# Kernel optimization log

Hardware: AMD Instinct MI355X
Metric: run time of the kernel (lower is better)

The kernel has to match this reference:

```python
import jax, jax.numpy as jnp
import numpy as np

D_MODEL = 1024
N_HEADS = 16
DIM_HEAD = D_MODEL // N_HEADS
SCALE = DIM_HEAD ** (-0.5)
B, T = 8, 1024


def setup_inputs() -> dict:
    key = jax.random.key(0)
    k1, k2, k3 = jax.random.split(key, 3)
    x = jax.random.normal(k1, (B, T, D_MODEL), dtype=jnp.float32)
    m = jnp.ones((B, T), dtype=jnp.float32)  # padding mask (1 = keep)
    w_qkv = jax.random.normal(k2, (3 * D_MODEL, D_MODEL), dtype=jnp.float32) * (D_MODEL ** -0.5)
    w_out = jax.random.normal(k3, (D_MODEL, D_MODEL), dtype=jnp.float32) * (D_MODEL ** -0.5)
    b_out = jnp.zeros((D_MODEL,), dtype=jnp.float32)
    return {"x": x, "m": m, "w_qkv": w_qkv, "w_out": w_out, "b_out": b_out, "l": T}


def reference(x, m, w_qkv, w_out, b_out, l):
    b, t, dm = x.shape
    qkv = jnp.einsum('btd,ed->bte', x, w_qkv)  # (b,t,3*d_model)
    q, k, v = jnp.split(qkv, 3, axis=-1)
    rs = lambda a: a.reshape(b, t, N_HEADS, DIM_HEAD)
    q, k, v = rs(q), rs(k), rs(v)
    e = jnp.einsum('bihd,bjhd->bijh', q, k) * SCALE  # (b,i,j,h)
    # combined padding + causal mask
    kpm = m[:, :, None] * m[:, None, :]              # (b,i,j)
    kpm = jnp.tril(kpm)[..., None]                   # (b,i,j,1)
    neg = -jnp.finfo(e.dtype).max
    e = jnp.where(kpm == 0, neg, e)
    a = jax.nn.softmax(e, axis=2)                    # softmax over j
    o = jnp.einsum('bijh,bjhd->bihd', a, v).reshape(b, t, dm)
    o = jnp.einsum('btd,ed->bte', o, w_out) + b_out
    # dropout is identity in eval mode
    return o * m[..., None]
```

## Files before the change

### kernel.cpp

```cpp
#include <hip/hip_runtime.h>
#include <cstdint>
#include <cstddef>

typedef unsigned short u16;
typedef __bf16 bf16;
typedef bf16 __attribute__((ext_vector_type(2))) bf16x2;
typedef bf16 __attribute__((ext_vector_type(8))) bf16x8;
typedef float __attribute__((ext_vector_type(4))) f32x4;
typedef u16 __attribute__((ext_vector_type(8))) u16x8;

#define QSCALE 0.18033688011112042f

__device__ __forceinline__ u16 f2b(float x) {
  unsigned u = __float_as_uint(x);
  unsigned r = (u + 0x7fffu + ((u >> 16) & 1u)) >> 16;
  return (u16)r;
}

__device__ __forceinline__ void gl_lds16(const void* g, void* lds) {
  __builtin_amdgcn_global_load_lds(
      (const __attribute__((address_space(1))) unsigned int*)g,
      (__attribute__((address_space(3))) unsigned int*)lds, 16, 0, 0);
}

__device__ __forceinline__ bf16x8 frag(const u16* base, int row, int kchunk) {
  const int c = kchunk ^ (row & 7);
  return *(const bf16x8*)(base + row * 64 + c * 8);
}
__device__ __forceinline__ void stage_tile4(const u16* gbase, int K, char* lbase,
                                            int wave, int lane) {
#pragma unroll
  for (int i = 0; i < 4; ++i) {
    const int q = wave * 64 + lane + i * 256;
    const int r = q >> 3, c = (q & 7) ^ (r & 7);
    gl_lds16(gbase + (size_t)r * K + c * 8, lbase + i * 4096 + wave * 1024);
  }
}

__device__ __forceinline__ bf16x8 frag32(const u16* base, int row, int kchunk) {
  const int c = kchunk ^ ((row >> 1) & 3);
  return *(const bf16x8*)(base + row * 32 + c * 8);
}
__device__ __forceinline__ void stage32(const u16* gbase, int K, char* lbase,
                                        int wave, int lane) {
  const int q0 = wave * 64 + lane;
  const int r0 = q0 >> 2, c0 = (q0 & 3) ^ ((r0 >> 1) & 3);
  gl_lds16(gbase + (size_t)r0 * K + c0 * 8, lbase + wave * 1024);
  const int q1 = q0 + 256;
  const int r1 = q1 >> 2, c1 = (q1 & 3) ^ ((r1 >> 1) & 3);
  gl_lds16(gbase + (size_t)r1 * K + c1 * 8, lbase + 4096 + wave * 1024);
}

__global__ __launch_bounds__(256) void castk(const float* __restrict__ in,
                                             u16* __restrict__ out, int n) {
  int i = (blockIdx.x * 256 + threadIdx.x) * 8;
  if (i >= n) return;
  float4 a = *(const float4*)(in + i);
  float4 b = *(const float4*)(in + i + 4);
  u16x8 v;
  v[0] = f2b(a.x); v[1] = f2b(a.y); v[2] = f2b(a.z); v[3] = f2b(a.w);
  v[4] = f2b(b.x); v[5] = f2b(b.y); v[6] = f2b(b.z); v[7] = f2b(b.w);
  *(u16x8*)(out + i) = v;
}

__global__ __launch_bounds__(256, 3) void gemm_qkv(
    const u16* __restrict__ A, const u16* __restrict__ B,
    u16* __restrict__ Qo, u16* __restrict__ Ko, u16* __restrict__ Vo) {
  __shared__ u16 As[3][128 * 32];
  __shared__ u16 Bs[3][128 * 32];
  const int tid = threadIdx.x;
  const int lane = tid & 63, wave = tid >> 6;
  const int fr = lane & 15, fg = lane >> 4;
  const int wr = wave >> 1, wc = wave & 1;
  const int bid = blockIdx.x;
  const int bm = bid & 63, bn = bid >> 6;
  const int K = 1024;
  const u16* Ab = A + (size_t)bm * 128 * K;
  const u16* Bb = B + (size_t)bn * 128 * K;

  f32x4 acc[4][4] = {};

  stage32(Ab, K, (char*)&As[0][0], wave, lane);
  stage32(Bb, K, (char*)&Bs[0][0], wave, lane);
  stage32(Ab + 32, K, (char*)&As[1][0], wave, lane);
  stage32(Bb + 32, K, (char*)&Bs[1][0], wave, lane);

  int cur = 0;
#pragma unroll 1
  for (int t = 0; t < 32; ++t) {
    if (t == 31) asm volatile("s_waitcnt vmcnt(0) lgkmcnt(0)" ::: "memory");
    else         asm volatile("s_waitcnt vmcnt(4) lgkmcnt(0)" ::: "memory");
    __builtin_amdgcn_s_barrier();
    __builtin_amdgcn_sched_barrier(0);
    if (t + 2 < 32) {
      int stg = cur + 2; if (stg >= 3) stg -= 3;
      stage32(Ab + (size_t)(t + 2) * 32, K, (char*)&As[stg][0], wave, lane);
      stage32(Bb + (size_t)(t + 2) * 32, K, (char*)&Bs[stg][0], wave, lane);
    }
    bf16x8 af[4], bfv[4];
#pragma unroll
    for (int mi = 0; mi < 4; ++mi)
      af[mi] = frag32(&As[cur][0], wr * 64 + mi * 16 + fr, fg);
#pragma unroll
    for (int ni = 0; ni < 4; ++ni)
      bfv[ni] = frag32(&Bs[cur][0], wc * 64 + ni * 16 + fr, fg);
#pragma unroll
    for (int mi = 0; mi < 4; ++mi)
#pragma unroll
      for (int ni = 0; ni < 4; ++ni)
        acc[mi][ni] = __builtin_amdgcn_mfma_f32_16x16x32_bf16(
            af[mi], bfv[ni], acc[mi][ni], 0, 0, 0);
    cur = (cur + 1 == 3) ? 0 : cur + 1;
  }

  const int gr0 = bm * 128 + wr * 64;
  const int gc0 = bn * 128 + wc * 64;
#pragma unroll
  for (int mi = 0; mi < 4; ++mi) {
    const int rb = gr0 + mi * 16 + fg * 4;
    const int b = rb >> 10, t = rb & 1023;
#pragma unroll
    for (int ni = 0; ni < 4; ++ni) {
      const int c = gc0 + ni * 16 + fr;
      const int region = c >> 10, cc = c & 1023;
      const int h = cc >> 6, d = cc & 63;
      const size_t bh = (size_t)(b * 16 + h);
      if (region == 0) {
#pragma unroll
        for (int g = 0; g < 4; ++g)
          Qo[(bh * 1024 + t + g) * 64 + d] = f2b(acc[mi][ni][g] * QSCALE);
      } else if (region == 1) {
#pragma unroll
        for (int g = 0; g < 4; ++g)
          Ko[(bh * 1024 + t + g) * 64 + d] = f2b(acc[mi][ni][g]);
      } else {
        ushort4 pv;
        pv.x = f2b(acc[mi][ni][0]);
        pv.y = f2b(acc[mi][ni][1]);
        pv.z = f2b(acc[mi][ni][2]);
        pv.w = f2b(acc[mi][ni][3]);
        *(ushort4*)(Vo + (bh * 64 + d) * 1024 + t) = pv;
      }
    }
  }
}

__global__ __launch_bounds__(256) void gemm_bt2(
    const u16* __restrict__ A, const u16* __restrict__ B,
    float* __restrict__ Co, const float* __restrict__ bias,
    const float* __restrict__ msk) {
  __shared__ u16 As[2][128 * 64];
  __shared__ u16 Bs[2][128 * 64];
  const int tid = threadIdx.x;
  const int lane = tid & 63, wave = tid >> 6;
  const int fr = lane & 15, fg = lane >> 4;
  const int wr = wave >> 1, wc = wave & 1;
  const int bid = blockIdx.x;
  const int bm = bid & 63, bn = bid >> 6;
  const int K = 1024, N = 1024;
  const u16* Ab = A + (size_t)bm * 128 * K;
  const u16* Bb = B + (size_t)bn * 128 * K;

  f32x4 acc[4][4] = {};

  stage_tile4(Ab, K, (char*)&As[0][0], wave, lane);
  stage_tile4(Bb, K, (char*)&Bs[0][0], wave, lane);
  __syncthreads();

  int cur = 0;
#pragma unroll 1
  for (int t = 0; t < 16; ++t) {
    if (t < 15) {
      stage_tile4(Ab + (size_t)(t + 1) * 64, K, (char*)&As[cur ^ 1][0], wave, lane);
      stage_tile4(Bb + (size_t)(t + 1) * 64, K, (char*)&Bs[cur ^ 1][0], wave, lane);
    }
    bf16x8 af[4][2], bfv[4][2];
#pragma unroll
    for (int mi = 0; mi < 4; ++mi)
#pragma unroll
      for (int kk = 0; kk < 2; ++kk)
        af[mi][kk] = frag(&As[cur][0], wr * 64 + mi * 16 + fr, kk * 4 + fg);
#pragma unroll
    for (int ni = 0; ni < 4; ++ni)
#pragma unroll
      for (int kk = 0; kk < 2; ++kk)
        bfv[ni][kk] = frag(&Bs[cur][0], wc * 64 + ni * 16 + fr, kk * 4 + fg);
#pragma unroll
    for (int mi = 0; mi < 4; ++mi)
#pragma unroll
      for (int ni = 0; ni < 4; ++ni)
#pragma unroll
        for (int kk = 0; kk < 2; ++kk)
          acc[mi][ni] = __builtin_amdgcn_mfma_f32_16x16x32_bf16(
              af[mi][kk], bfv[ni][kk], acc[mi][ni], 0, 0, 0);
    __syncthreads();
    cur ^= 1;
  }

  const int gr0 = bm * 128 + wr * 64;
  const int gc0 = bn * 128 + wc * 64;
#pragma unroll
  for (int mi = 0; mi < 4; ++mi) {
    const int rb = gr0 + mi * 16 + fg * 4;
#pragma unroll
    for (int ni = 0; ni < 4; ++ni) {
      const int c = gc0 + ni * 16 + fr;
      const float bo = bias[c];
#pragma unroll
      for (int g = 0; g < 4; ++g) {
        const int r = rb + g;
        Co[(size_t)r * N + c] = (acc[mi][ni][g] + bo) * msk[r];
      }
    }
  }
}

__global__ __launch_bounds__(256) void attnk(const u16* __restrict__ Qb,
                                             const u16* __restrict__ Kb,
                                             const u16* __restrict__ Vtb,
                                             const float* __restrict__ msk,
                                             u16* __restrict__ Ob) {
  __shared__ u16 Ks[2][64 * 64];
  __shared__ u16 Vs[2][64 * 64];
  __shared__ float mlds[1024];
  __shared__ int allone;
  const int tid = threadIdx.x;
  const int lane = tid & 63, wave = tid >> 6;
  const int fr = lane & 15, fg = lane >> 4;
  const int bid = blockIdx.x;
  const int s = bid >> 7;
  const int bh = bid & 127;
  const int b = bh >> 4, h = bh & 15;

  const float4 mv = ((const float4*)(msk + (size_t)b * 1024))[tid];
  ((float4*)mlds)[tid] = mv;
  if (tid == 0) allone = 1;
  __syncthreads();
  if (mv.x != 1.f || mv.y != 1.f || mv.z != 1.f || mv.w != 1.f) allone = 0;

  auto stage = [&](int kb, int buf) {
    const int q0 = wave * 64 + lane;
    const int r0 = q0 >> 3, c0 = (q0 & 7) ^ (r0 & 7);
    gl_lds16(Kb + ((size_t)bh * 1024 + kb * 64 + r0) * 64 + c0 * 8,
             (char*)&Ks[buf][0] + wave * 1024);
    gl_lds16(Vtb + ((size_t)bh * 64 + r0) * 1024 + kb * 64 + c0 * 8,
             (char*)&Vs[buf][0] + wave * 1024);
    const int q1 = q0 + 256;
    const int r1 = q1 >> 3, c1 = (q1 & 7) ^ (r1 & 7);
    gl_lds16(Kb + ((size_t)bh * 1024 + kb * 64 + r1) * 64 + c1 * 8,
             (char*)&Ks[buf][0] + 4096 + wave * 1024);
    gl_lds16(Vtb + ((size_t)bh * 64 + r1) * 1024 + kb * 64 + c1 * 8,
             (char*)&Vs[buf][0] + 4096 + wave * 1024);
  };

  int qw = s * 64 + wave * 16;
  bf16x8 qf[2];
  auto loadQ = [&]() {
#pragma unroll
    for (int kc = 0; kc < 2; ++kc)
      qf[kc] = *(const bf16x8*)(Qb + ((size_t)bh * 1024 + qw + fr) * 64 +
                                kc * 32 + fg * 8);
  };
  loadQ();

  f32x4 o[4] = {};
  float mrun = -3.0e38f, lrun = 0.f;

  auto writeO = [&]() {
    const float inv = 1.0f / lrun;
#pragma unroll
    for (int g = 0; g < 4; ++g) {
      const float invr = __shfl(inv, fg * 4 + g);
      const int q = qw + fg * 4 + g;
#pragma unroll
      for (int dt = 0; dt < 4; ++dt)
        Ob[((size_t)b * 1024 + q) * 1024 + h * 64 + dt * 16 + fr] =
            f2b(o[dt][g] * invr);
    }
  };

  stage(0, 0);

#pragma unroll 1
  for (int it = 0; it <= 16; ++it) {
    __syncthreads();
    const bool mfast = __builtin_amdgcn_readfirstlane(allone) != 0;
    if (it < 16) {
      const int nkb = (it + 1 <= s) ? (it + 1) : (it - s);
      stage(nkb, (it + 1) & 1);
    }
    if (it == s + 1) {
      writeO();
      qw = (15 - s) * 64 + wave * 16;
      loadQ();
#pragma unroll
      for (int dt = 0; dt < 4; ++dt) o[dt] = f32x4{0.f, 0.f, 0.f, 0.f};
      mrun = -3.0e38f;
      lrun = 0.f;
    }
    const int kb = (it <= s) ? it : (it - s - 1);
    const u16* Kc = &Ks[it & 1][0];
    const u16* Vc = &Vs[it & 1][0];

    f32x4 st[4];
    const f32x4 z = {0.f, 0.f, 0.f, 0.f};
    bf16x8 kf0[4], kf1[4];
#pragma unroll
    for (int nt = 0; nt < 4; ++nt) {
      const int krow = nt * 16 + fr;
      const int cb0r = (0 * 4 + fg) ^ (krow & 7);
      const int cb1r = (1 * 4 + fg) ^ (krow & 7);
      kf0[nt] = *(const bf16x8*)(Kc + krow * 64 + cb0r * 8);
      kf1[nt] = *(const bf16x8*)(Kc + krow * 64 + cb1r * 8);
    }
    __builtin_amdgcn_s_setprio(1);
#pragma unroll
    for (int nt = 0; nt < 4; ++nt) {
      st[nt] = __builtin_amdgcn_mfma_f32_16x16x32_bf16(kf0[nt], qf[0], z, 0, 0, 0);
      st[nt] = __builtin_amdgcn_mfma_f32_16x16x32_bf16(kf1[nt], qf[1], st[nt], 0, 0, 0);
    }
    __builtin_amdgcn_s_setprio(0);

    if (kb * 64 + 63 > qw) {
      const int q = qw + fr;
#pragma unroll
      for (int nt = 0; nt < 4; ++nt)
#pragma unroll
        for (int g = 0; g < 4; ++g) {
          const int j = kb * 64 + nt * 16 + fg * 4 + g;
          if (j > q) st[nt][g] = -3.0e38f;
        }
    }

    float mx = st[0][0];
#pragma unroll
    for (int nt = 0; nt < 4; ++nt)
#pragma unroll
      for (int g = 0; g < 4; ++g) mx = fmaxf(mx, st[nt][g]);
    mx = fmaxf(mx, __shfl_xor(mx, 16));
    mx = fmaxf(mx, __shfl_xor(mx, 32));
    float nm, sc;
    int doR;
    if (__all(mx <= mrun + 8.f)) {
      nm = mrun; sc = 1.f; doR = 0;
    } else {
      nm = fmaxf(mrun, mx);
      sc = exp2f(mrun - nm);
      mrun = nm; doR = 1;
    }
    float rs = 0.f;
    if (mfast) {
#pragma unroll
      for (int nt = 0; nt < 4; ++nt)
#pragma unroll
        for (int g = 0; g < 4; ++g) {
          const float pq = exp2f(st[nt][g] - nm);
          st[nt][g] = pq;
          rs += pq;
        }
    } else {
      float kmv[4][4];
#pragma unroll
      for (int nt = 0; nt < 4; ++nt) {
        const float4 km4 = *(const float4*)(&mlds[kb * 64 + nt * 16 + fg * 4]);
        kmv[nt][0] = km4.x; kmv[nt][1] = km4.y; kmv[nt][2] = km4.z; kmv[nt][3] = km4.w;
      }
#pragma unroll
      for (int nt = 0; nt < 4; ++nt)
#pragma unroll
        for (int g = 0; g < 4; ++g) {
          const float pq = exp2f(st[nt][g] - nm) * kmv[nt][g];
          st[nt][g] = pq;
          rs += pq;
        }
    }
    rs += __shfl_xor(rs, 16);
    rs += __shfl_xor(rs, 32);
    lrun = doR ? (lrun * sc + rs) : (lrun + rs);

    int pk[4][2];
#pragma unroll
    for (int nt = 0; nt < 4; ++nt)
#pragma unroll
      for (int hh = 0; hh < 2; ++hh) {
        bf16x2 tp;
        tp[0] = (bf16)st[nt][2 * hh];
        tp[1] = (bf16)st[nt][2 * hh + 1];
        pk[nt][hh] = __builtin_bit_cast(int, tp);
      }

    bf16x8 pa[2];
#pragma unroll
    for (int jc = 0; jc < 2; ++jc) {
      int w[4];
#pragma unroll
      for (int e2 = 0; e2 < 4; ++e2) {
        const int sl = fr + ((fg & 1) << 5) + ((e2 & 2) ? 16 : 0);
        const int lo = __shfl(pk[jc * 2 + 0][e2 & 1], sl);
        const int hi = __shfl(pk[jc * 2 + 1][e2 & 1], sl);
        w[e2] = (fg & 2) ? hi : lo;
      }
      int4 wi = {w[0], w[1], w[2], w[3]};
      pa[jc] = __builtin_bit_cast(bf16x8, wi);
    }

    if (doR) {
#pragma unroll
      for (int g = 0; g < 4; ++g) {
        const float scr = __shfl(sc, fg * 4 + g);
#pragma unroll
        for (int dt = 0; dt < 4; ++dt) o[dt][g] *= scr;
      }
    }

    __builtin_amdgcn_s_setprio(1);
#pragma unroll
    for (int jc = 0; jc < 2; ++jc)
#pragma unroll
      for (int dt = 0; dt < 4; ++dt) {
        const int vrow = dt * 16 + fr;
        const int cb = (jc * 4 + fg) ^ (vrow & 7);
        const bf16x8 vf = *(const bf16x8*)(Vc + vrow * 64 + cb * 8);
        o[dt] = __builtin_amdgcn_mfma_f32_16x16x32_bf16(pa[jc], vf, o[dt], 0, 0, 0);
      }
    __builtin_amdgcn_s_setprio(0);
  }

  writeO();
}

extern "C" void kernel_launch(void* const* d_in, const int* in_sizes, int n_in,
                              void* d_out, int out_size, void* d_ws, size_t ws_size,
                              hipStream_t stream) {
  (void)in_sizes; (void)n_in; (void)out_size; (void)ws_size;
  const float* x = (const float*)d_in[0];
  const float* m = (const float*)d_in[1];
  const float* w_qkv = (const float*)d_in[2];
  const float* w_out = (const float*)d_in[3];
  const float* b_out = (const float*)d_in[4];
  float* out = (float*)d_out;

  char* ws = (char*)d_ws;
  const size_t MB = 1u << 20;
  u16* Xb    = (u16*)(ws + 0);
  u16* Wqkvb = (u16*)(ws + 16 * MB);
  u16* Woutb = (u16*)(ws + 22 * MB);
  u16* Qb    = (u16*)(ws + 24 * MB);
  u16* Kb    = (u16*)(ws + 40 * MB);
  u16* Vtb   = (u16*)(ws + 56 * MB);
  u16* Ob    = Xb;

  castk<<<4096, 256, 0, stream>>>(x, Xb, 8 * 1024 * 1024);
  castk<<<1536, 256, 0, stream>>>(w_qkv, Wqkvb, 3072 * 1024);
  castk<<<512, 256, 0, stream>>>(w_out, Woutb, 1024 * 1024);

  gemm_qkv<<<1536, 256, 0, stream>>>(Xb, Wqkvb, Qb, Kb, Vtb);

  attnk<<<1024, 256, 0, stream>>>(Qb, Kb, Vtb, m, Ob);

  gemm_bt2<<<512, 256, 0, stream>>>(Ob, Woutb, out, b_out, m);
}
```

Baseline: 155.4 us.

## Merge cast kernels, enlarge QKV GEMM tile to 256x256, defer attention max shuffle

Three separate fp32-to-bf16 cast launches become one kernel that dispatches on block index, removing two launches. The QKV projection GEMM goes from 128x128 tiles with 256 threads to 256x256 tiles with 512 threads, giving more operand reuse per LDS load and fewer blocks (384). In attention, the cross-lane max reduction is skipped when every lane's local max stays within the threshold of the running max. The larger GEMM tile raises accumulator registers and LDS per block, which may lower occupancy. With only 384 blocks there may also be tail imbalance across CUs.

```diff
diff --git a/kernel.cpp b/kernel.cpp
--- a/kernel.cpp
+++ b/kernel.cpp
@@ -41,20 +41,21 @@
   const int c = kchunk ^ ((row >> 1) & 3);
   return *(const bf16x8*)(base + row * 32 + c * 8);
 }
-__device__ __forceinline__ void stage32(const u16* gbase, int K, char* lbase,
-                                        int wave, int lane) {
-  const int q0 = wave * 64 + lane;
-  const int r0 = q0 >> 2, c0 = (q0 & 3) ^ ((r0 >> 1) & 3);
-  gl_lds16(gbase + (size_t)r0 * K + c0 * 8, lbase + wave * 1024);
-  const int q1 = q0 + 256;
-  const int r1 = q1 >> 2, c1 = (q1 & 3) ^ ((r1 >> 1) & 3);
-  gl_lds16(gbase + (size_t)r1 * K + c1 * 8, lbase + 4096 + wave * 1024);
-}
-
-__global__ __launch_bounds__(256) void castk(const float* __restrict__ in,
-                                             u16* __restrict__ out, int n) {
-  int i = (blockIdx.x * 256 + threadIdx.x) * 8;
-  if (i >= n) return;
+
+__global__ __launch_bounds__(256) void castk3(const float* __restrict__ x,
+                                              const float* __restrict__ wq,
+                                              const float* __restrict__ wo,
+                                              u16* __restrict__ xb,
+                                              u16* __restrict__ wqb,
+                                              u16* __restrict__ wob) {
+  const int blk = blockIdx.x;
+  const float* in;
+  u16* out;
+  int base;
+  if (blk < 4096)      { in = x;  out = xb;  base = blk; }
+  else if (blk < 5632) { in = wq; out = wqb; base = blk - 4096; }
+  else                 { in = wo; out = wob; base = blk - 5632; }
+  const int i = (base * 256 + threadIdx.x) * 8;
   float4 a = *(const float4*)(in + i);
   float4 b = *(const float4*)(in + i + 4);
   u16x8 v;
@@ -63,27 +64,36 @@
   *(u16x8*)(out + i) = v;
 }
 
-__global__ __launch_bounds__(256, 3) void gemm_qkv(
+__global__ __launch_bounds__(512, 2) void gemm_qkv(
     const u16* __restrict__ A, const u16* __restrict__ B,
     u16* __restrict__ Qo, u16* __restrict__ Ko, u16* __restrict__ Vo) {
-  __shared__ u16 As[3][128 * 32];
-  __shared__ u16 Bs[3][128 * 32];
+  __shared__ u16 As[3][256 * 32];
+  __shared__ u16 Bs[3][256 * 32];
   const int tid = threadIdx.x;
   const int lane = tid & 63, wave = tid >> 6;
   const int fr = lane & 15, fg = lane >> 4;
-  const int wr = wave >> 1, wc = wave & 1;
+  const int wm = wave >> 2, wn = wave & 3;
   const int bid = blockIdx.x;
-  const int bm = bid & 63, bn = bid >> 6;
+  const int bm = bid & 31, bn = bid >> 5;
   const int K = 1024;
-  const u16* Ab = A + (size_t)bm * 128 * K;
-  const u16* Bb = B + (size_t)bn * 128 * K;
-
-  f32x4 acc[4][4] = {};
-
-  stage32(Ab, K, (char*)&As[0][0], wave, lane);
-  stage32(Bb, K, (char*)&Bs[0][0], wave, lane);
-  stage32(Ab + 32, K, (char*)&As[1][0], wave, lane);
-  stage32(Bb + 32, K, (char*)&Bs[1][0], wave, lane);
+  const u16* Ab = A + (size_t)bm * 256 * K;
+  const u16* Bb = B + (size_t)bn * 256 * K;
+
+  f32x4 acc[8][4] = {};
+
+  auto stage = [&](const u16* gbase, char* lbase) {
+    const int q0 = wave * 64 + lane;
+    const int r0 = q0 >> 2, c0 = (q0 & 3) ^ ((r0 >> 1) & 3);
+    gl_lds16(gbase + (size_t)r0 * K + c0 * 8, lbase + wave * 1024);
+    const int q1 = q0 + 512;
+    const int r1 = q1 >> 2, c1 = (q1 & 3) ^ ((r1 >> 1) & 3);
+    gl_lds16(gbase + (size_t)r1 * K + c1 * 8, lbase + 8192 + wave * 1024);
+  };
+
+  stage(Ab, (char*)&As[0][0]);
+  stage(Bb, (char*)&Bs[0][0]);
+  stage(Ab + 32, (char*)&As[1][0]);
+  stage(Bb + 32, (char*)&Bs[1][0]);
 
   int cur = 0;
 #pragma unroll 1
@@ -94,29 +104,28 @@
     __builtin_amdgcn_sched_barrier(0);
     if (t + 2 < 32) {
       int stg = cur + 2; if (stg >= 3) stg -= 3;
-      stage32(Ab + (size_t)(t + 2) * 32, K, (char*)&As[stg][0], wave, lane);
-      stage32(Bb + (size_t)(t + 2) * 32, K, (char*)&Bs[stg][0], wave, lane);
-    }
-    bf16x8 af[4], bfv[4];
-#pragma unroll
-    for (int mi = 0; mi < 4; ++mi)
-      af[mi] = frag32(&As[cur][0], wr * 64 + mi * 16 + fr, fg);
+      stage(Ab + (size_t)(t + 2) * 32, (char*)&As[stg][0]);
+      stage(Bb + (size_t)(t + 2) * 32, (char*)&Bs[stg][0]);
+    }
+    bf16x8 bfv[4];
 #pragma unroll
     for (int ni = 0; ni < 4; ++ni)
-      bfv[ni] = frag32(&Bs[cur][0], wc * 64 + ni * 16 + fr, fg);
-#pragma unroll
-    for (int mi = 0; mi < 4; ++mi)
+      bfv[ni] = frag32(&Bs[cur][0], wn * 64 + ni * 16 + fr, fg);
+#pragma unroll
+    for (int mi = 0; mi < 8; ++mi) {
+      const bf16x8 af = frag32(&As[cur][0], wm * 128 + mi * 16 + fr, fg);
 #pragma unroll
       for (int ni = 0; ni < 4; ++ni)
         acc[mi][ni] = __builtin_amdgcn_mfma_f32_16x16x32_bf16(
-            af[mi], bfv[ni], acc[mi][ni], 0, 0, 0);
+            af, bfv[ni], acc[mi][ni], 0, 0, 0);
+    }
     cur = (cur + 1 == 3) ? 0 : cur + 1;
   }
 
-  const int gr0 = bm * 128 + wr * 64;
-  const int gc0 = bn * 128 + wc * 64;
-#pragma unroll
-  for (int mi = 0; mi < 4; ++mi) {
+  const int gr0 = bm * 256 + wm * 128;
+  const int gc0 = bn * 256 + wn * 64;
+#pragma unroll
+  for (int mi = 0; mi < 8; ++mi) {
     const int rb = gr0 + mi * 16 + fg * 4;
     const int b = rb >> 10, t = rb & 1023;
 #pragma unroll
@@ -332,18 +341,18 @@
         }
     }
 
-    float mx = st[0][0];
+    float mxl = st[0][0];
 #pragma unroll
     for (int nt = 0; nt < 4; ++nt)
 #pragma unroll
-      for (int g = 0; g < 4; ++g) mx = fmaxf(mx, st[nt][g]);
-    mx = fmaxf(mx, __shfl_xor(mx, 16));
-    mx = fmaxf(mx, __shfl_xor(mx, 32));
+      for (int g = 0; g < 4; ++g) mxl = fmaxf(mxl, st[nt][g]);
     float nm, sc;
     int doR;
-    if (__all(mx <= mrun + 8.f)) {
+    if (__all(mxl <= mrun + 8.f)) {
       nm = mrun; sc = 1.f; doR = 0;
     } else {
+      float mx = fmaxf(mxl, __shfl_xor(mxl, 16));
+      mx = fmaxf(mx, __shfl_xor(mx, 32));
       nm = fmaxf(mrun, mx);
       sc = exp2f(mrun - nm);
       mrun = nm; doR = 1;
@@ -450,11 +459,9 @@
   u16* Vtb   = (u16*)(ws + 56 * MB);
   u16* Ob    = Xb;
 
-  castk<<<4096, 256, 0, stream>>>(x, Xb, 8 * 1024 * 1024);
-  castk<<<1536, 256, 0, stream>>>(w_qkv, Wqkvb, 3072 * 1024);
-  castk<<<512, 256, 0, stream>>>(w_out, Woutb, 1024 * 1024);
-
-  gemm_qkv<<<1536, 256, 0, stream>>>(Xb, Wqkvb, Qb, Kb, Vtb);
+  castk3<<<6144, 256, 0, stream>>>(x, w_qkv, w_out, Xb, Wqkvb, Woutb);
+
+  gemm_qkv<<<384, 512, 0, stream>>>(Xb, Wqkvb, Qb, Kb, Vtb);
 
   attnk<<<1024, 256, 0, stream>>>(Qb, Kb, Vtb, m, Ob);
 
```

Result: slower. 175.1 us (+12.7%).
